# Kernel tuning notes

Measured on AMD Instinct MI355X. Metric: run time of the kernel, lower is better.

Reference implementation:

```python
import jax, jax.numpy as jnp
import numpy as np

B, IN, OUT, P = 512, 4096, 4096, 4
BITS = 4
MAX_INT = float(2 ** (BITS - 1) - 1)  # 7.0


def setup_inputs() -> dict:
    key = jax.random.key(0)
    k1, k2, k3, k4 = jax.random.split(key, 4)
    x = jax.random.normal(k1, (B, IN), dtype=jnp.float32)
    # Cached LFSR-generated pseudo-random matrix, values normalized to [-1, 1]
    U = jax.random.uniform(k2, (OUT * IN, P), dtype=jnp.float32, minval=-1.0, maxval=1.0)
    # 4-bit quantized projection: integers in [-7, 7] stored as float
    q = jnp.round(jnp.clip(jax.random.normal(k3, (P,), dtype=jnp.float32) * 3.0, -MAX_INT, MAX_INT))
    b = jax.random.normal(k4, (OUT,), dtype=jnp.float32)
    return {"x": x, "U": U, "q": q, "b": b, "exponent": 0}


def reference(x, U, q, b, exponent):
    # dequantize: t_hat = q / max_int * 2^exponent  (shared-exponent 4-bit dequant)
    scale = jnp.float32(2.0) ** exponent
    t_hat = q / MAX_INT * scale                      # [P]
    # reconstruct full weight: W = U @ t_hat, reshape to (out, in)
    w = (U @ t_hat).reshape(OUT, IN)                 # [OUT, IN]
    # original layer forward (nn.Linear): y = x @ W^T + b
    return x @ w.T + b                               # [B, OUT]
```

## Files before the change

### kernel.cpp

```cpp
#include <hip/hip_runtime.h>
#include <hip/hip_bf16.h>

typedef unsigned short ushort_t;
typedef unsigned int uint_t;
typedef __attribute__((ext_vector_type(4))) float f32x4;
typedef __attribute__((ext_vector_type(8))) short bf16x8;

#define B_DIM 512
#define IN_DIM 4096
#define OUT_DIM 4096
#define BM 128
#define BN 128
#define BK 32
#define KSPLIT 8

__device__ __forceinline__ ushort_t f2bf(float f) {
    union { float f; uint_t u; } v; v.f = f;
    uint_t r = v.u + 0x7fffu + ((v.u >> 16) & 1u);
    return (ushort_t)(r >> 16);
}

__device__ __forceinline__ void async_copy16(void* lds, const void* g) {
    __builtin_amdgcn_global_load_lds(
        (const __attribute__((address_space(1))) uint_t*)g,
        (__attribute__((address_space(3))) uint_t*)lds, 16, 0, 0);
}

__global__ __launch_bounds__(256) void build_w(const float4* __restrict__ U4,
                                               const float* __restrict__ q,
                                               const int* __restrict__ expo,
                                               ushort_t* __restrict__ Wb) {
    const float scale = exp2f((float)expo[0]) * (1.0f / 7.0f);
    const float t0 = q[0] * scale, t1 = q[1] * scale,
                t2 = q[2] * scale, t3 = q[3] * scale;
    size_t i = (size_t)blockIdx.x * 256 + threadIdx.x;
    float4 u = U4[i];
    Wb[i] = f2bf(u.x * t0 + u.y * t1 + u.z * t2 + u.w * t3);
}

__global__ __launch_bounds__(256) void conv_x(const float4* __restrict__ X4,
                                              ushort_t* __restrict__ Xb) {
    size_t i = (size_t)blockIdx.x * 256 + threadIdx.x;
    float4 a = X4[i];
    ushort_t r[4] = { f2bf(a.x), f2bf(a.y), f2bf(a.z), f2bf(a.w) };
    *(uint2*)(Xb + i * 4) = *(const uint2*)r;
}

__global__ __launch_bounds__(256, 4) void gemm_splitk(
    const ushort_t* __restrict__ A,
    const ushort_t* __restrict__ Bm,
    float* __restrict__ part)
{
    const int M = B_DIM, N = OUT_DIM, K = IN_DIM;
    __shared__ ushort_t sA[BM * BK];
    __shared__ ushort_t sB[BN * BK];

    const int tid  = threadIdx.x;
    const int lane = tid & 63;
    const int wave = tid >> 6;
    const int wr = (wave >> 1) * 64;
    const int wc = (wave & 1) * 64;

    const int m0 = blockIdx.y * BM;
    const int n0 = blockIdx.x * BN;
    const int kseg  = K / KSPLIT;
    const size_t kbase = (size_t)blockIdx.z * kseg;

    const int srow = tid >> 2;
    const int scol = (tid & 3) * 8;
    const ushort_t* ga0 = A  + (size_t)(m0 + srow) * K + kbase + scol;
    const ushort_t* ga1 = ga0 + (size_t)64 * K;
    const ushort_t* gb0 = Bm + (size_t)(n0 + srow) * K + kbase + scol;
    const ushort_t* gb1 = gb0 + (size_t)64 * K;
    ushort_t* la = sA + tid * 8;
    ushort_t* lb = sB + tid * 8;

    const int quad = lane >> 4;
    const int r16  = lane & 15;
    const ushort_t* fa = sA + (wr + r16) * BK + quad * 8;
    const ushort_t* fb = sB + (wc + r16) * BK + quad * 8;

    f32x4 acc[4][4] = {};

    const int nsteps = kseg / BK;
    for (int s = 0; s < nsteps; ++s) {
        async_copy16(la,        ga0);
        async_copy16(la + 2048, ga1);
        async_copy16(lb,        gb0);
        async_copy16(lb + 2048, gb1);
        ga0 += BK; ga1 += BK; gb0 += BK; gb1 += BK;
        __syncthreads();

        bf16x8 av[4], bv[4];
#pragma unroll
        for (int i = 0; i < 4; ++i) {
            av[i] = *(const bf16x8*)(fa + i * 16 * BK);
            bv[i] = *(const bf16x8*)(fb + i * 16 * BK);
        }
#pragma unroll
        for (int i = 0; i < 4; ++i)
#pragma unroll
            for (int j = 0; j < 4; ++j)
                acc[i][j] = __builtin_amdgcn_mfma_f32_16x16x32_bf16(
                    av[i], bv[j], acc[i][j], 0, 0, 0);
        __syncthreads();
    }

    float* outp = part + (size_t)blockIdx.z * M * N;
#pragma unroll
    for (int i = 0; i < 4; ++i) {
        const int mrow = m0 + wr + i * 16 + quad * 4;
#pragma unroll
        for (int j = 0; j < 4; ++j) {
            const int ncol = n0 + wc + j * 16 + r16;
            float* o = outp + (size_t)mrow * N + ncol;
#pragma unroll
            for (int r = 0; r < 4; ++r)
                o[(size_t)r * N] = acc[i][j][r];
        }
    }
}

__global__ __launch_bounds__(256) void reduce_bias(const float4* __restrict__ part,
                                                   const float4* __restrict__ bias,
                                                   float4* __restrict__ out) {
    const int MN4 = (B_DIM * OUT_DIM) / 4;
    int i = blockIdx.x * 256 + threadIdx.x;
    float4 bb = bias[i & 1023];
    float sx = bb.x, sy = bb.y, sz = bb.z, sw = bb.w;
#pragma unroll
    for (int k = 0; k < KSPLIT; ++k) {
        float4 p = part[i + (size_t)k * MN4];
        sx += p.x; sy += p.y; sz += p.z; sw += p.w;
    }
    float4 o; o.x = sx; o.y = sy; o.z = sz; o.w = sw;
    out[i] = o;
}

extern "C" void kernel_launch(void* const* d_in, const int* in_sizes, int n_in,
                              void* d_out, int out_size, void* d_ws, size_t ws_size,
                              hipStream_t stream) {
    const float* x    = (const float*)d_in[0];
    const float* U    = (const float*)d_in[1];
    const float* q    = (const float*)d_in[2];
    const float* b    = (const float*)d_in[3];
    const int*   expo = (const int*)d_in[4];
    float* out = (float*)d_out;

    char* ws = (char*)d_ws;
    ushort_t* Wb  = (ushort_t*)ws;
    ushort_t* Xb  = (ushort_t*)(ws + 33554432);
    float*    prt = (float*)(ws + 37748736);

    build_w<<<65536, 256, 0, stream>>>((const float4*)U, q, expo, Wb);
    conv_x<<<2048, 256, 0, stream>>>((const float4*)x, Xb);
    gemm_splitk<<<dim3(32, 4, KSPLIT), 256, 0, stream>>>(Xb, Wb, prt);
    reduce_bias<<<2048, 256, 0, stream>>>((const float4*)prt, (const float4*)b,
                                          (float4*)out);
}
```

Measured before the change: 415.3 us.

## Fuse weight reconstruction into split-K GEMM, each block covering full batch

Removes the separate kernel that built the bf16 weight matrix. The GEMM now reads U directly, computes the dequantized projection per tile and stores it to LDS. Blocks cover all 512 batch rows with a 32-column output tile, so U is streamed exactly once and the intermediate weight write and its repeated re-reads go away. The trade-off is synchronous, unpipelined global loads of U inside the K loop, plus a large A tile in LDS that reduces occupancy.

```diff
diff --git a/kernel.cpp b/kernel.cpp
--- a/kernel.cpp
+++ b/kernel.cpp
@@ -9,8 +9,7 @@
 #define B_DIM 512
 #define IN_DIM 4096
 #define OUT_DIM 4096
-#define BM 128
-#define BN 128
+#define BN 32
 #define BK 32
 #define KSPLIT 8
 
@@ -26,18 +25,6 @@
         (__attribute__((address_space(3))) uint_t*)lds, 16, 0, 0);
 }
 
-__global__ __launch_bounds__(256) void build_w(const float4* __restrict__ U4,
-                                               const float* __restrict__ q,
-                                               const int* __restrict__ expo,
-                                               ushort_t* __restrict__ Wb) {
-    const float scale = exp2f((float)expo[0]) * (1.0f / 7.0f);
-    const float t0 = q[0] * scale, t1 = q[1] * scale,
-                t2 = q[2] * scale, t3 = q[3] * scale;
-    size_t i = (size_t)blockIdx.x * 256 + threadIdx.x;
-    float4 u = U4[i];
-    Wb[i] = f2bf(u.x * t0 + u.y * t1 + u.z * t2 + u.w * t3);
-}
-
 __global__ __launch_bounds__(256) void conv_x(const float4* __restrict__ X4,
                                               ushort_t* __restrict__ Xb) {
     size_t i = (size_t)blockIdx.x * 256 + threadIdx.x;
@@ -46,73 +33,75 @@
     *(uint2*)(Xb + i * 4) = *(const uint2*)r;
 }
 
-__global__ __launch_bounds__(256, 4) void gemm_splitk(
+__global__ __launch_bounds__(256, 3) void gemm_fused(
     const ushort_t* __restrict__ A,
-    const ushort_t* __restrict__ Bm,
+    const float4* __restrict__ U4,
+    const float* __restrict__ q,
+    const int* __restrict__ expo,
     float* __restrict__ part)
 {
     const int M = B_DIM, N = OUT_DIM, K = IN_DIM;
-    __shared__ ushort_t sA[BM * BK];
-    __shared__ ushort_t sB[BN * BK];
+    __shared__ ushort_t sA[B_DIM * BK];
+    __shared__ ushort_t sW[BN * BK];
 
     const int tid  = threadIdx.x;
     const int lane = tid & 63;
     const int wave = tid >> 6;
-    const int wr = (wave >> 1) * 64;
-    const int wc = (wave & 1) * 64;
 
-    const int m0 = blockIdx.y * BM;
     const int n0 = blockIdx.x * BN;
-    const int kseg  = K / KSPLIT;
-    const size_t kbase = (size_t)blockIdx.z * kseg;
+    const int kseg = K / KSPLIT;
+    const size_t kbase = (size_t)blockIdx.y * kseg;
 
-    const int srow = tid >> 2;
-    const int scol = (tid & 3) * 8;
-    const ushort_t* ga0 = A  + (size_t)(m0 + srow) * K + kbase + scol;
-    const ushort_t* ga1 = ga0 + (size_t)64 * K;
-    const ushort_t* gb0 = Bm + (size_t)(n0 + srow) * K + kbase + scol;
-    const ushort_t* gb1 = gb0 + (size_t)64 * K;
-    ushort_t* la = sA + tid * 8;
-    ushort_t* lb = sB + tid * 8;
+    const float scale = exp2f((float)expo[0]) * (1.0f / 7.0f);
+    const float t0 = q[0] * scale, t1 = q[1] * scale,
+                t2 = q[2] * scale, t3 = q[3] * scale;
+
+    const ushort_t* gA = A + (size_t)(wave * 128 + (lane >> 2)) * K + kbase + (lane & 3) * 8;
+    ushort_t* lA = sA + wave * 128 * BK + lane * 8;
+
+    const float4* gU = U4 + (size_t)(n0 + (tid >> 3)) * K + kbase + (tid & 7) * 4;
+    ushort_t* lW = sW + (tid >> 3) * BK + (tid & 7) * 4;
 
     const int quad = lane >> 4;
     const int r16  = lane & 15;
-    const ushort_t* fa = sA + (wr + r16) * BK + quad * 8;
-    const ushort_t* fb = sB + (wc + r16) * BK + quad * 8;
+    const ushort_t* fa = sA + (wave * 128 + r16) * BK + quad * 8;
+    const ushort_t* fb = sW + r16 * BK + quad * 8;
 
-    f32x4 acc[4][4] = {};
+    f32x4 acc[8][2] = {};
 
     const int nsteps = kseg / BK;
     for (int s = 0; s < nsteps; ++s) {
-        async_copy16(la,        ga0);
-        async_copy16(la + 2048, ga1);
-        async_copy16(lb,        gb0);
-        async_copy16(lb + 2048, gb1);
-        ga0 += BK; ga1 += BK; gb0 += BK; gb1 += BK;
+#pragma unroll
+        for (int c = 0; c < 8; ++c)
+            async_copy16(lA + c * 16 * BK, gA + (size_t)c * 16 * K);
+        float4 u0 = gU[0], u1 = gU[1], u2 = gU[2], u3 = gU[3];
+        gA += BK; gU += BK;
+        ushort_t wq[4];
+        wq[0] = f2bf(u0.x * t0 + u0.y * t1 + u0.z * t2 + u0.w * t3);
+        wq[1] = f2bf(u1.x * t0 + u1.y * t1 + u1.z * t2 + u1.w * t3);
+        wq[2] = f2bf(u2.x * t0 + u2.y * t1 + u2.z * t2 + u2.w * t3);
+        wq[3] = f2bf(u3.x * t0 + u3.y * t1 + u3.z * t2 + u3.w * t3);
+        *(uint2*)lW = *(const uint2*)wq;
         __syncthreads();
 
-        bf16x8 av[4], bv[4];
+        bf16x8 bv0 = *(const bf16x8*)(fb);
+        bf16x8 bv1 = *(const bf16x8*)(fb + 16 * BK);
 #pragma unroll
-        for (int i = 0; i < 4; ++i) {
-            av[i] = *(const bf16x8*)(fa + i * 16 * BK);
-            bv[i] = *(const bf16x8*)(fb + i * 16 * BK);
+        for (int i = 0; i < 8; ++i) {
+            bf16x8 av = *(const bf16x8*)(fa + i * 16 * BK);
+            acc[i][0] = __builtin_amdgcn_mfma_f32_16x16x32_bf16(av, bv0, acc[i][0], 0, 0, 0);
+            acc[i][1] = __builtin_amdgcn_mfma_f32_16x16x32_bf16(av, bv1, acc[i][1], 0, 0, 0);
         }
-#pragma unroll
-        for (int i = 0; i < 4; ++i)
-#pragma unroll
-            for (int j = 0; j < 4; ++j)
-                acc[i][j] = __builtin_amdgcn_mfma_f32_16x16x32_bf16(
-                    av[i], bv[j], acc[i][j], 0, 0, 0);
         __syncthreads();
     }
 
-    float* outp = part + (size_t)blockIdx.z * M * N;
+    float* outp = part + (size_t)blockIdx.y * M * N;
 #pragma unroll
-    for (int i = 0; i < 4; ++i) {
-        const int mrow = m0 + wr + i * 16 + quad * 4;
+    for (int i = 0; i < 8; ++i) {
+        const int mrow = wave * 128 + i * 16 + quad * 4;
 #pragma unroll
-        for (int j = 0; j < 4; ++j) {
-            const int ncol = n0 + wc + j * 16 + r16;
+        for (int j = 0; j < 2; ++j) {
+            const int ncol = n0 + j * 16 + r16;
             float* o = outp + (size_t)mrow * N + ncol;
 #pragma unroll
             for (int r = 0; r < 4; ++r)
@@ -148,13 +137,11 @@
     float* out = (float*)d_out;
 
     char* ws = (char*)d_ws;
-    ushort_t* Wb  = (ushort_t*)ws;
-    ushort_t* Xb  = (ushort_t*)(ws + 33554432);
-    float*    prt = (float*)(ws + 37748736);
+    ushort_t* Xb  = (ushort_t*)ws;
+    float*    prt = (float*)(ws + 4194304);
 
-    build_w<<<65536, 256, 0, stream>>>((const float4*)U, q, expo, Wb);
     conv_x<<<2048, 256, 0, stream>>>((const float4*)x, Xb);
-    gemm_splitk<<<dim3(32, 4, KSPLIT), 256, 0, stream>>>(Xb, Wb, prt);
+    gemm_fused<<<dim3(128, KSPLIT), 256, 0, stream>>>(Xb, (const float4*)U, q, expo, prt);
     reduce_bias<<<2048, 256, 0, stream>>>((const float4*)prt, (const float4*)b,
                                           (float4*)out);
 }
```

New measurement: 431.0 us. 1.04x slower.
